# Kernel optimization log

Hardware: AMD Instinct MI355X
Metric: run time of the kernel (lower is better)

The kernel has to match this reference:

```python
import jax, jax.numpy as jnp
import numpy as np

H = 64          # hidden_size / SINDy latent dim
DM = 128        # d_model (GRU input size)
FF = 128        # dim_feedforward
NL = 2          # num_sindy_layers
EPS = 1e-5      # LayerNorm eps (torch default)
TRI_I, TRI_J = np.triu_indices(H)          # poly_order=2 pairs, torch loop order (i<=j)
LIB = 1 + H + TRI_I.size                   # 2145


def layernorm(x, g, b):
    m = jnp.mean(x, axis=-1, keepdims=True)
    v = jnp.mean((x - m) ** 2, axis=-1, keepdims=True)
    return (x - m) * jax.lax.rsqrt(v + EPS) * g + b


def sindy_library(z):
    # z: (N, H) -> Theta: (N, 1 + H + H*(H+1)/2); same term ordering as torch loops
    ones = jnp.ones((z.shape[0], 1), z.dtype)
    quad = z[:, TRI_I] * z[:, TRI_J]
    return jnp.concatenate([ones, z, quad], axis=1)


def gru_layer(x, Wih, Whh, bih, bhh):
    # x: (B, S, in), Wih: (3H, in), Whh: (3H, H); torch GRU gate order r,z,n
    xp = jnp.einsum('bsi,gi->bsg', x, Wih) + bih  # (B,S,3H) precomputed input projections
    B = x.shape[0]

    def step(h, xpt):
        gh = h @ Whh.T + bhh
        r = jax.nn.sigmoid(xpt[:, :H] + gh[:, :H])
        z = jax.nn.sigmoid(xpt[:, H:2 * H] + gh[:, H:2 * H])
        n = jnp.tanh(xpt[:, 2 * H:] + r * gh[:, 2 * H:])
        h = (1.0 - z) * n + z * h
        return h, h

    h0 = jnp.zeros((B, H), x.dtype)
    _, ys = jax.lax.scan(step, h0, jnp.swapaxes(xp, 0, 1))  # scan over time
    return jnp.swapaxes(ys, 0, 1)  # (B, S, H)


def sindy_layer(src, coef, g1, b1n, W1, bf1, W2, bf2, g2, b2n):
    B, S, _ = src.shape
    theta = sindy_library(src.reshape(-1, H))          # (N, LIB)
    upd = (theta @ coef).reshape(B, S, H)              # (B, S, H)
    src = layernorm(src + upd, g1, b1n)                # dropout = identity (eval)
    ff = jax.nn.gelu(src @ W1.T + bf1, approximate=False) @ W2.T + bf2
    return layernorm(src + ff, g2, b2n)


def setup_inputs() -> dict:
    key = jax.random.key(0)
    ks = jax.random.split(key, 24)
    f = lambda k, sh, s=0.05: (jax.random.normal(k, sh, dtype=jnp.float32) * s)
    inp = {
        'x': jax.random.normal(ks[0], (32, 500, DM), dtype=jnp.float32),
        # GRU layer 0 (input DM) and layer 1 (input H)
        'Wih0': f(ks[1], (3 * H, DM)), 'Whh0': f(ks[2], (3 * H, H)),
        'bih0': f(ks[3], (3 * H,)), 'bhh0': f(ks[4], (3 * H,)),
        'Wih1': f(ks[5], (3 * H, H)), 'Whh1': f(ks[6], (3 * H, H)),
        'bih1': f(ks[7], (3 * H,)), 'bhh1': f(ks[8], (3 * H,)),
        # stacked params for NL=2 identical SINDy layers
        'coeffs': f(ks[9], (NL, LIB, H), 0.02),
        'ln1_g': jnp.ones((NL, H), jnp.float32), 'ln1_b': jnp.zeros((NL, H), jnp.float32),
        'W1': f(ks[10], (NL, FF, H)), 'b1': f(ks[11], (NL, FF)),
        'W2': f(ks[12], (NL, H, FF)), 'b2': f(ks[13], (NL, H)),
        'ln2_g': jnp.ones((NL, H), jnp.float32), 'ln2_b': jnp.zeros((NL, H), jnp.float32),
    }
    return inp


def reference(x, Wih0, Whh0, bih0, bhh0, Wih1, Whh1, bih1, bhh1,
              coeffs, ln1_g, ln1_b, W1, b1, W2, b2, ln2_g, ln2_b):
    h = gru_layer(x, Wih0, Whh0, bih0, bhh0)
    h = gru_layer(h, Wih1, Whh1, bih1, bhh1)
    for l in range(NL):
        h = sindy_layer(h, coeffs[l], ln1_g[l], ln1_b[l], W1[l], b1[l],
                        W2[l], b2[l], ln2_g[l], ln2_b[l])
    return h, h[:, -1, :]
```

## Files before the change

kernel.cpp:

```cpp
#include <hip/hip_runtime.h>
#include <hip/hip_bf16.h>
#include <math.h>

#define H 64
#define DM 128
#define GDIM 192
#define BSZ 32
#define SEQ 500
#define NROW (BSZ*SEQ)
#define LIBN 2145
#define FFD 128
#define NKC2 75
#define NGRP 300
#define CPK2 153600

typedef __attribute__((ext_vector_type(8))) short short8;
typedef __attribute__((ext_vector_type(4))) float f32x4;
typedef __attribute__((ext_vector_type(2))) float f32x2;
typedef __attribute__((ext_vector_type(4))) unsigned u32x4;

__device__ __forceinline__ float sigf(float x) {
    return 1.0f / (1.0f + __expf(-x));
}
__device__ __forceinline__ float tanhfast(float x) {
    x = fminf(fmaxf(x, -15.0f), 15.0f);
    float t = __expf(-2.0f * x);
    return (1.0f - t) / (1.0f + t);
}
__device__ __forceinline__ short bf16r(float f) {
    unsigned u = __float_as_uint(f);
    unsigned r = (u + 0x7fffu + ((u >> 16) & 1u)) >> 16;
    return (short)r;
}
__device__ __forceinline__ f32x2 pkfma(f32x2 a, f32x2 b, f32x2 c) {
    f32x2 d;
    asm("v_pk_fma_f32 %0, %1, %2, %3" : "=v"(d) : "v"(a), "v"(b), "v"(c));
    return d;
}

__device__ __forceinline__ void grp_decode(int g, int& a, int& b) {
    if (g < 8) { a = 64; b = g * 8; }
    else if (g == 8 || g >= 297) { a = 64; b = 64; }
    else {
        int G = g - 9, acc = 0;
        a = 0; b = 0;
        for (int i2 = 0; i2 < 64; i2++) {
            int cnt = 8 - (i2 >> 3);
            if (G < acc + cnt) { a = i2; b = ((i2 >> 3) + (G - acc)) * 8; break; }
            acc += cnt;
        }
    }
}

__global__ void pack_all(const float* __restrict__ wih0,
                         const float* __restrict__ coeffs,
                         const float* __restrict__ w1,
                         const float* __restrict__ w2,
                         float* __restrict__ wtp,
                         short* __restrict__ bfa) {
    int idx = blockIdx.x * 256 + threadIdx.x;
    if (idx < GDIM * DM) {
        int e  = idx & 3;
        int g  = (idx >> 2) % GDIM;
        int k4 = idx / (GDIM * 4);
        wtp[idx] = wih0[g * DM + k4 * 4 + e];
        return;
    }
    int r = idx - GDIM * DM;
    int l = r / (CPK2 + 2 * 8192);
    int q = r % (CPK2 + 2 * 8192);
    if (q < CPK2) {
        const float* coef = coeffs + (size_t)l * LIBN * H;
        int j = q & 7, lane = (q >> 3) & 63, nt = (q >> 9) & 3, kc = q >> 11;
        int grp = kc * 4 + (lane >> 4);
        int row = -1;
        if (grp < 8) row = 1 + grp * 8 + j;
        else if (grp == 8) row = (j == 0) ? 0 : -1;
        else if (grp < 297) {
            int a, b;
            grp_decode(grp, a, b);
            int jdx = b + j;
            if (jdx >= a) row = 65 + a * 64 - (a * (a - 1)) / 2 + (jdx - a);
        }
        int c = nt * 16 + (lane & 15);
        bfa[(size_t)l * CPK2 + q] = (row >= 0) ? bf16r(coef[(size_t)row * H + c]) : (short)0;
        return;
    }
    int q2 = q - CPK2;
    if (q2 < 8192) {
        const float* w1l = w1 + (size_t)l * FFD * H;
        int j = q2 & 7, lane = (q2 >> 3) & 63, nt = (q2 >> 9) & 7, kc = q2 >> 12;
        int k = kc * 32 + ((lane >> 4) << 3) + j;
        int n = nt * 16 + (lane & 15);
        bfa[(size_t)2 * CPK2 + l * 8192 + q2] = bf16r(w1l[(size_t)n * H + k]);
        return;
    }
    int q3 = q2 - 8192;
    const float* w2l = w2 + (size_t)l * H * FFD;
    int j = q3 & 7, lane = (q3 >> 3) & 63, nt = (q3 >> 9) & 3, kc = q3 >> 11;
    int k = kc * 32 + ((lane >> 4) << 3) + j;
    int n = nt * 16 + (lane & 15);
    bfa[(size_t)2 * CPK2 + 2 * 8192 + l * 8192 + q3] = bf16r(w2l[(size_t)n * FFD + k]);
}

__global__ __launch_bounds__(192, 2) void xp0_gemm(const float* __restrict__ x,
                                                   const float* __restrict__ wtp,
                                                   const float* __restrict__ bih0,
                                                   float* __restrict__ xpT) {
    __shared__ float xs[64][DM];
    int rb = blockIdx.x * 64;
    for (int idx = threadIdx.x; idx < 64 * 32; idx += 192) {
        int r = idx >> 5, k4 = idx & 31;
        ((f32x4*)xs[r])[k4] = ((const f32x4*)(x + (size_t)(rb + r) * DM))[k4];
    }
    __syncthreads();
    int g = threadIdx.x;
    float bias = bih0[g];
    float acc[64];
#pragma unroll
    for (int r = 0; r < 64; r++) acc[r] = bias;
    for (int k4 = 0; k4 < 32; k4++) {
        f32x4 w4 = ((const f32x4*)wtp)[k4 * GDIM + g];
#pragma unroll
        for (int r = 0; r < 64; r++) {
            f32x4 xv = ((f32x4*)xs[r])[k4];
            acc[r] += w4[0] * xv[0] + w4[1] * xv[1] + w4[2] * xv[2] + w4[3] * xv[3];
        }
    }
    for (int r = 0; r < 64; r++) {
        int row = rb + r;
        int bb = row / 500;
        int ss = row - bb * 500;
        xpT[(((size_t)bb * 125 + (ss >> 2)) * GDIM + g) * 4 + (ss & 3)] = acc[r];
    }
}

__global__ __launch_bounds__(768, 3) void gru_fused(const float* __restrict__ xpT,
                                                    const float* __restrict__ whh0,
                                                    const float* __restrict__ bhh0,
                                                    const float* __restrict__ wih1,
                                                    const float* __restrict__ bih1,
                                                    const float* __restrict__ whh1,
                                                    const float* __restrict__ bhh1,
                                                    float* __restrict__ hbuf) {
    int b = blockIdx.x;
    int tid = threadIdx.x;
    int wv = __builtin_amdgcn_readfirstlane(tid >> 6);
    int lane = tid & 63;
    int m = wv % 3;
    int q = wv / 3;
    int k0 = q * 16;

    __shared__ __align__(16) float h0s[H];
    __shared__ __align__(16) float h1s[H];
    __shared__ float part[3][4][GDIM];

    if (tid < H) { h0s[tid] = 0.0f; h1s[tid] = 0.0f; }

    const float* W = (m == 0) ? whh0 : (m == 1) ? wih1 : whh1;
    f32x2 wrp[8], wzp[8], wnp[8];
#pragma unroll
    for (int k4 = 0; k4 < 4; k4++) {
        f32x4 a = ((const f32x4*)(W + (size_t)lane * H + k0))[k4];
        f32x4 c = ((const f32x4*)(W + (size_t)(H + lane) * H + k0))[k4];
        f32x4 d = ((const f32x4*)(W + (size_t)(2 * H + lane) * H + k0))[k4];
        wrp[2*k4]   = __builtin_shufflevector(a, a, 0, 1);
        wrp[2*k4+1] = __builtin_shufflevector(a, a, 2, 3);
        wzp[2*k4]   = __builtin_shufflevector(c, c, 0, 1);
        wzp[2*k4+1] = __builtin_shufflevector(c, c, 2, 3);
        wnp[2*k4]   = __builtin_shufflevector(d, d, 0, 1);
        wnp[2*k4+1] = __builtin_shufflevector(d, d, 2, 3);
    }

    float b0r = 0, b0z = 0, b0n = 0;
    float b1ir = 0, b1iz = 0, b1in = 0, b1hr = 0, b1hz = 0, b1hn = 0;
    float hreg0 = 0.0f, hreg1 = 0.0f;
    float hb4[4] = {0.f, 0.f, 0.f, 0.f};
    f32x4 xc[4][3];
    const float* xpB = xpT + (size_t)b * 125 * GDIM * 4;

    if (wv == 0) {
        b0r = bhh0[lane]; b0z = bhh0[H + lane]; b0n = bhh0[2 * H + lane];
#pragma unroll
        for (int g3 = 0; g3 < 3; g3++) {
            xc[0][g3] = *(const f32x4*)(xpB + ((size_t)0 * GDIM + g3 * 64 + lane) * 4);
            xc[1][g3] = *(const f32x4*)(xpB + ((size_t)1 * GDIM + g3 * 64 + lane) * 4);
        }
    } else if (wv == 2) {
        b1ir = bih1[lane]; b1iz = bih1[H + lane]; b1in = bih1[2 * H + lane];
        b1hr = bhh1[lane]; b1hz = bhh1[H + lane]; b1hn = bhh1[2 * H + lane];
    }
    __syncthreads();

    auto loadch = [&](int c, int buf) {
        if (c < 125) {
#pragma unroll
            for (int g3 = 0; g3 < 3; g3++)
                xc[buf][g3] = *(const f32x4*)(xpB + ((size_t)c * GDIM + g3 * 64 + lane) * 4);
        }
    };

    auto step = [&](int s, int e, float xr, float xz, float xn) {
        const float* hv = (m == 2) ? h1s : h0s;
        f32x2 arp = {0.f, 0.f}, azp = {0.f, 0.f}, anp = {0.f, 0.f};
#pragma unroll
        for (int t4 = 0; t4 < 4; t4++) {
            f32x4 h4 = ((const f32x4*)(hv + k0))[t4];
            f32x2 hlo = __builtin_shufflevector(h4, h4, 0, 1);
            f32x2 hhi = __builtin_shufflevector(h4, h4, 2, 3);
            arp = pkfma(wrp[2*t4], hlo, arp);
            arp = pkfma(wrp[2*t4+1], hhi, arp);
            azp = pkfma(wzp[2*t4], hlo, azp);
            azp = pkfma(wzp[2*t4+1], hhi, azp);
            anp = pkfma(wnp[2*t4], hlo, anp);
            anp = pkfma(wnp[2*t4+1], hhi, anp);
        }
        part[m][q][lane] = arp[0] + arp[1];
        part[m][q][H + lane] = azp[0] + azp[1];
        part[m][q][2 * H + lane] = anp[0] + anp[1];
        __syncthreads();

        if (wv == 0) {
            if (s < SEQ) {
                float gr = b0r, gz = b0z, gn = b0n;
#pragma unroll
                for (int qq = 0; qq < 4; qq++) {
                    gr += part[0][qq][lane];
                    gz += part[0][qq][H + lane];
                    gn += part[0][qq][2 * H + lane];
                }
                float rg = sigf(xr + gr);
                float zg = sigf(xz + gz);
                float ng = tanhfast(xn + rg * gn);
                hreg0 = (1.0f - zg) * ng + zg * hreg0;
                h0s[lane] = hreg0;
            }
        } else if (wv == 2) {
            if (s >= 1) {
                float xr1 = b1ir, xz1 = b1iz, xn1 = b1in;
                float gr1 = b1hr, gz1 = b1hz, gn1 = b1hn;
#pragma unroll
                for (int qq = 0; qq < 4; qq++) {
                    xr1 += part[1][qq][lane];
                    xz1 += part[1][qq][H + lane];
                    xn1 += part[1][qq][2 * H + lane];
                    gr1 += part[2][qq][lane];
                    gz1 += part[2][qq][H + lane];
                    gn1 += part[2][qq][2 * H + lane];
                }
                float rg = sigf(xr1 + gr1);
                float zg = sigf(xz1 + gz1);
                float ng = tanhfast(xn1 + rg * gn1);
                hreg1 = (1.0f - zg) * ng + zg * hreg1;
                h1s[lane] = hreg1;
                hb4[(e + 3) & 3] = hreg1;
                if (e == 0) {
                    float* dst = hbuf + ((size_t)b * SEQ + (s - 4)) * H + lane;
#pragma unroll
                    for (int t = 0; t < 4; t++) dst[t * H] = hb4[t];
                }
            }
        }
        __syncthreads();
    };

    for (int scb = 0; scb < 31; scb++) {
#pragma unroll
        for (int sci = 0; sci < 4; sci++) {
            int sc = scb * 4 + sci;
            if (wv == 0 && (sci & 1) == 0) {
                loadch(sc + 2, (sci + 2) & 3);
                loadch(sc + 3, (sci + 3) & 3);
            }
            int s0 = sc * 4;
            step(s0 + 0, 0, xc[sci][0][0], xc[sci][1][0], xc[sci][2][0]);
            step(s0 + 1, 1, xc[sci][0][1], xc[sci][1][1], xc[sci][2][1]);
            step(s0 + 2, 2, xc[sci][0][2], xc[sci][1][2], xc[sci][2][2]);
            step(s0 + 3, 3, xc[sci][0][3], xc[sci][1][3], xc[sci][2][3]);
        }
    }
    {
        step(496, 0, xc[0][0][0], xc[0][1][0], xc[0][2][0]);
        step(497, 1, xc[0][0][1], xc[0][1][1], xc[0][2][1]);
        step(498, 2, xc[0][0][2], xc[0][1][2], xc[0][2][2]);
        step(499, 3, xc[0][0][3], xc[0][1][3], xc[0][2][3]);
    }
    step(500, 0, 0.0f, 0.0f, 0.0f);
}

__global__ __launch_bounds__(512) void sindy_mfma(float* __restrict__ hbuf,
                                                  const short* __restrict__ cpk,
                                                  const short* __restrict__ w1p,
                                                  const short* __restrict__ w2p,
                                                  const float* __restrict__ g1,
                                                  const float* __restrict__ b1n,
                                                  const float* __restrict__ bf1,
                                                  const float* __restrict__ bf2v,
                                                  const float* __restrict__ g2,
                                                  const float* __restrict__ b2n,
                                                  float* __restrict__ out,
                                                  int final_layer) {
    __shared__ float z[65 * 68];
    __shared__ float upd[64 * 68];
    __shared__ float ff[64 * 132];
    __shared__ unsigned kmap2[NGRP];
    __shared__ float bfs1[FFD], bfs2[H], g1s[H], b1s[H], g2s[H], b2s[H];

    int tid = threadIdx.x;
    int wv = __builtin_amdgcn_readfirstlane(tid >> 6);
    int lane = tid & 63;
    int row0 = blockIdx.x * 64;

    for (int idx = tid; idx < 64 * 16; idx += 512) {
        int r = idx >> 4, c4 = idx & 15;
        *(f32x4*)&z[r * 68 + c4 * 4] = *(const f32x4*)&hbuf[(size_t)(row0 + r) * H + c4 * 4];
    }
    for (int idx = tid; idx < 64 * 17; idx += 512)
        *(f32x4*)&upd[idx * 4] = (f32x4){0.f, 0.f, 0.f, 0.f};
    if (tid < 64) {
        z[tid * 68 + 64] = 1.0f; z[tid * 68 + 65] = 0.0f;
        z[tid * 68 + 66] = 0.0f; z[tid * 68 + 67] = 0.0f;
    }
    if (tid < 68) z[64 * 68 + tid] = 0.0f;
    if (tid < NGRP) {
        int a, b;
        grp_decode(tid, a, b);
        kmap2[tid] = ((unsigned)a << 16) | (unsigned)b;
    }
    if (tid < FFD) bfs1[tid] = bf1[tid];
    if (tid < H) {
        bfs2[tid] = bf2v[tid];
        g1s[tid] = g1[tid]; b1s[tid] = b1n[tid];
        g2s[tid] = g2[tid]; b2s[tid] = b2n[tid];
    }
    __syncthreads();

    int kj0 = ((lane >> 4) << 3);
    int m0 = (wv & 3) * 16;
    int m = m0 + (lane & 15);
    int rbase = m0 + ((lane >> 4) << 2);
    int cb16 = lane & 15;
    const float* zrow = &z[m * 68];

    {
        int p = wv >> 2;
        f32x4 acc[4] = {{0,0,0,0},{0,0,0,0},{0,0,0,0},{0,0,0,0}};
        for (int kc = p; kc < NKC2; kc += 2) {
            unsigned ab = kmap2[kc * 4 + (lane >> 4)];
            float za = zrow[ab >> 16];
            const float* zb = &zrow[ab & 0xffffu];
            f32x4 z0 = *(const f32x4*)zb;
            f32x4 z1 = *(const f32x4*)(zb + 4);
            short8 af;
            af[0] = bf16r(za * z0[0]);
            af[1] = bf16r(za * z0[1]);
            af[2] = bf16r(za * z0[2]);
            af[3] = bf16r(za * z0[3]);
            af[4] = bf16r(za * z1[0]);
            af[5] = bf16r(za * z1[1]);
            af[6] = bf16r(za * z1[2]);
            af[7] = bf16r(za * z1[3]);
            const short* cb = cpk + ((size_t)(kc * 4) * 64 + lane) * 8;
#pragma unroll
            for (int nt = 0; nt < 4; nt++) {
                short8 bf = *(const short8*)(cb + (size_t)nt * 512);
                acc[nt] = __builtin_amdgcn_mfma_f32_16x16x32_bf16(af, bf, acc[nt], 0, 0, 0);
            }
        }
#pragma unroll
        for (int nt = 0; nt < 4; nt++)
#pragma unroll
            for (int r = 0; r < 4; r++)
                atomicAdd(&upd[(rbase + r) * 68 + nt * 16 + cb16], acc[nt][r]);
    }
    __syncthreads();

    if (wv == 0) {
        float v[64];
        float s1 = 0.0f;
#pragma unroll
        for (int c = 0; c < 64; c++) { v[c] = z[lane * 68 + c] + upd[lane * 68 + c]; s1 += v[c]; }
        float mn = s1 * (1.0f / 64.0f);
        float s2 = 0.0f;
#pragma unroll
        for (int c = 0; c < 64; c++) { float d = v[c] - mn; s2 += d * d; }
        float rstd = 1.0f / sqrtf(s2 * (1.0f / 64.0f) + 1e-5f);
#pragma unroll
        for (int c = 0; c < 64; c++)
            z[lane * 68 + c] = (v[c] - mn) * rstd * g1s[c] + b1s[c];
    }
    __syncthreads();

    {
        int nq = wv >> 2;
        f32x4 acc[4] = {{0,0,0,0},{0,0,0,0},{0,0,0,0},{0,0,0,0}};
#pragma unroll
        for (int kc = 0; kc < 2; kc++) {
            f32x4 za = *(const f32x4*)&z[m * 68 + kc * 32 + kj0];
            f32x4 zb = *(const f32x4*)&z[m * 68 + kc * 32 + kj0 + 4];
            short8 af;
            af[0] = bf16r(za[0]); af[1] = bf16r(za[1]); af[2] = bf16r(za[2]); af[3] = bf16r(za[3]);
            af[4] = bf16r(zb[0]); af[5] = bf16r(zb[1]); af[6] = bf16r(zb[2]); af[7] = bf16r(zb[3]);
#pragma unroll
            for (int t = 0; t < 4; t++) {
                int nt = nq * 4 + t;
                short8 bf = *(const short8*)(w1p + ((size_t)(kc * 8 + nt) * 64 + lane) * 8);
                acc[t] = __builtin_amdgcn_mfma_f32_16x16x32_bf16(af, bf, acc[t], 0, 0, 0);
            }
        }
#pragma unroll
        for (int t = 0; t < 4; t++) {
            int col = (nq * 4 + t) * 16 + cb16;
#pragma unroll
            for (int r = 0; r < 4; r++) {
                float v = acc[t][r] + bfs1[col];
                ff[(rbase + r) * 132 + col] = 0.5f * v * (1.0f + erff(v * 0.70710678118654752f));
            }
        }
    }
    __syncthreads();

    {
        int nh = wv >> 2;
        f32x4 acc[2] = {{0,0,0,0},{0,0,0,0}};
        const float* frow = &ff[m * 132];
#pragma unroll
        for (int kc = 0; kc < 4; kc++) {
            f32x4 fa = *(const f32x4*)&frow[kc * 32 + kj0];
            f32x4 fb = *(const f32x4*)&frow[kc * 32 + kj0 + 4];
            short8 af;
            af[0] = bf16r(fa[0]); af[1] = bf16r(fa[1]); af[2] = bf16r(fa[2]); af[3] = bf16r(fa[3]);
            af[4] = bf16r(fb[0]); af[5] = bf16r(fb[1]); af[6] = bf16r(fb[2]); af[7] = bf16r(fb[3]);
#pragma unroll
            for (int t = 0; t < 2; t++) {
                int nt = nh * 2 + t;
                short8 bf = *(const short8*)(w2p + ((size_t)(kc * 4 + nt) * 64 + lane) * 8);
                acc[t] = __builtin_amdgcn_mfma_f32_16x16x32_bf16(af, bf, acc[t], 0, 0, 0);
            }
        }
#pragma unroll
        for (int t = 0; t < 2; t++) {
            int col = (nh * 2 + t) * 16 + cb16;
#pragma unroll
            for (int r = 0; r < 4; r++)
                upd[(rbase + r) * 68 + col] = acc[t][r] + bfs2[col];
        }
    }
    __syncthreads();

    if (wv == 0) {
        float v[64];
        float s1 = 0.0f;
#pragma unroll
        for (int c = 0; c < 64; c++) { v[c] = z[lane * 68 + c] + upd[lane * 68 + c]; s1 += v[c]; }
        float mn = s1 * (1.0f / 64.0f);
        float s2 = 0.0f;
#pragma unroll
        for (int c = 0; c < 64; c++) { float d = v[c] - mn; s2 += d * d; }
        float rstd = 1.0f / sqrtf(s2 * (1.0f / 64.0f) + 1e-5f);
        int row = row0 + lane;
#pragma unroll
        for (int c = 0; c < 64; c++) {
            float res = (v[c] - mn) * rstd * g2s[c] + b2s[c];
            if (!final_layer) {
                hbuf[(size_t)row * H + c] = res;
            } else {
                out[(size_t)row * H + c] = res;
                if (row % SEQ == SEQ - 1)
                    out[(size_t)NROW * H + (row / SEQ) * H + c] = res;
            }
        }
    }
}

extern "C" void kernel_launch(void* const* d_in, const int* in_sizes, int n_in,
                              void* d_out, int out_size, void* d_ws, size_t ws_size,
                              hipStream_t stream) {
    const float* x    = (const float*)d_in[0];
    const float* wih0 = (const float*)d_in[1];
    const float* whh0 = (const float*)d_in[2];
    const float* bih0 = (const float*)d_in[3];
    const float* bhh0 = (const float*)d_in[4];
    const float* wih1 = (const float*)d_in[5];
    const float* whh1 = (const float*)d_in[6];
    const float* bih1 = (const float*)d_in[7];
    const float* bhh1 = (const float*)d_in[8];
    const float* coeffs = (const float*)d_in[9];
    const float* ln1g = (const float*)d_in[10];
    const float* ln1b = (const float*)d_in[11];
    const float* w1   = (const float*)d_in[12];
    const float* b1   = (const float*)d_in[13];
    const float* w2   = (const float*)d_in[14];
    const float* b2   = (const float*)d_in[15];
    const float* ln2g = (const float*)d_in[16];
    const float* ln2b = (const float*)d_in[17];

    float* out = (float*)d_out;
    float* ws  = (float*)d_ws;
    float* xpT = ws;
    float* wtp = ws + (size_t)NROW * GDIM;
    short* bfa = (short*)(wtp + GDIM * DM);
    short* cpk[2] = { bfa, bfa + CPK2 };
    short* w1pk[2] = { bfa + 2 * CPK2, bfa + 2 * CPK2 + 8192 };
    short* w2pk[2] = { bfa + 2 * CPK2 + 2 * 8192, bfa + 2 * CPK2 + 3 * 8192 };
    float* hbuf = out;

    pack_all<<<1424, 256, 0, stream>>>(wih0, coeffs, w1, w2, wtp, bfa);
    xp0_gemm<<<NROW / 64, 192, 0, stream>>>(x, wtp, bih0, xpT);
    gru_fused<<<BSZ, 768, 0, stream>>>(xpT, whh0, bhh0, wih1, bih1, whh1, bhh1, hbuf);
    for (int l = 0; l < 2; l++) {
        sindy_mfma<<<NROW / 64, 512, 0, stream>>>(
            hbuf, cpk[l], w1pk[l], w2pk[l],
            ln1g + l * H, ln1b + l * H, b1 + l * FFD,
            b2 + l * H, ln2g + l * H, ln2b + l * H,
            out, l == 1);
    }
}
```

Measured before the change: 519.9 us.

## Fuse both SINDy layers into one kernel and parallelize LayerNorm across threads

Replaces the two per-layer SINDy launches with a single kernel that loops over both layers while keeping each 64-row tile resident in shared memory. This removes one kernel launch and the global write and re-read of the intermediate hidden state. LayerNorm is also rewritten so all 512 threads take part, eight per row with shuffle reductions, instead of only the first wave doing it serially. The cost is a longer kernel with extra barriers and an extra clearing of the update buffer between layers.

```diff
diff --git a/kernel.cpp b/kernel.cpp
--- a/kernel.cpp
+++ b/kernel.cpp
@@ -288,23 +288,21 @@
     step(500, 0, 0.0f, 0.0f, 0.0f);
 }
 
-__global__ __launch_bounds__(512) void sindy_mfma(float* __restrict__ hbuf,
-                                                  const short* __restrict__ cpk,
-                                                  const short* __restrict__ w1p,
-                                                  const short* __restrict__ w2p,
-                                                  const float* __restrict__ g1,
-                                                  const float* __restrict__ b1n,
-                                                  const float* __restrict__ bf1,
-                                                  const float* __restrict__ bf2v,
-                                                  const float* __restrict__ g2,
-                                                  const float* __restrict__ b2n,
-                                                  float* __restrict__ out,
-                                                  int final_layer) {
+__global__ __launch_bounds__(512) void sindy_fused(const float* __restrict__ hbuf_in,
+                                                   const short* __restrict__ bfa,
+                                                   const float* __restrict__ ln1g,
+                                                   const float* __restrict__ ln1b,
+                                                   const float* __restrict__ b1g,
+                                                   const float* __restrict__ b2g,
+                                                   const float* __restrict__ ln2g,
+                                                   const float* __restrict__ ln2b,
+                                                   float* __restrict__ out) {
     __shared__ float z[65 * 68];
     __shared__ float upd[64 * 68];
     __shared__ float ff[64 * 132];
     __shared__ unsigned kmap2[NGRP];
-    __shared__ float bfs1[FFD], bfs2[H], g1s[H], b1s[H], g2s[H], b2s[H];
+    __shared__ float bfs1[2][FFD], bfs2[2][H];
+    __shared__ float g1s[2][H], b1s[2][H], g2s[2][H], b2s[2][H];
 
     int tid = threadIdx.x;
     int wv = __builtin_amdgcn_readfirstlane(tid >> 6);
@@ -313,7 +311,7 @@
 
     for (int idx = tid; idx < 64 * 16; idx += 512) {
         int r = idx >> 4, c4 = idx & 15;
-        *(f32x4*)&z[r * 68 + c4 * 4] = *(const f32x4*)&hbuf[(size_t)(row0 + r) * H + c4 * 4];
+        *(f32x4*)&z[r * 68 + c4 * 4] = *(const f32x4*)&hbuf_in[(size_t)(row0 + r) * H + c4 * 4];
     }
     for (int idx = tid; idx < 64 * 17; idx += 512)
         *(f32x4*)&upd[idx * 4] = (f32x4){0.f, 0.f, 0.f, 0.f};
@@ -327,11 +325,13 @@
         grp_decode(tid, a, b);
         kmap2[tid] = ((unsigned)a << 16) | (unsigned)b;
     }
-    if (tid < FFD) bfs1[tid] = bf1[tid];
+    if (tid < FFD) { bfs1[0][tid] = b1g[tid]; bfs1[1][tid] = b1g[FFD + tid]; }
     if (tid < H) {
-        bfs2[tid] = bf2v[tid];
-        g1s[tid] = g1[tid]; b1s[tid] = b1n[tid];
-        g2s[tid] = g2[tid]; b2s[tid] = b2n[tid];
+        bfs2[0][tid] = b2g[tid];      bfs2[1][tid] = b2g[H + tid];
+        g1s[0][tid] = ln1g[tid];      g1s[1][tid] = ln1g[H + tid];
+        b1s[0][tid] = ln1b[tid];      b1s[1][tid] = ln1b[H + tid];
+        g2s[0][tid] = ln2g[tid];      g2s[1][tid] = ln2g[H + tid];
+        b2s[0][tid] = ln2b[tid];      b2s[1][tid] = ln2b[H + tid];
     }
     __syncthreads();
 
@@ -341,134 +341,163 @@
     int rbase = m0 + ((lane >> 4) << 2);
     int cb16 = lane & 15;
     const float* zrow = &z[m * 68];
-
-    {
-        int p = wv >> 2;
-        f32x4 acc[4] = {{0,0,0,0},{0,0,0,0},{0,0,0,0},{0,0,0,0}};
-        for (int kc = p; kc < NKC2; kc += 2) {
-            unsigned ab = kmap2[kc * 4 + (lane >> 4)];
-            float za = zrow[ab >> 16];
-            const float* zb = &zrow[ab & 0xffffu];
-            f32x4 z0 = *(const f32x4*)zb;
-            f32x4 z1 = *(const f32x4*)(zb + 4);
-            short8 af;
-            af[0] = bf16r(za * z0[0]);
-            af[1] = bf16r(za * z0[1]);
-            af[2] = bf16r(za * z0[2]);
-            af[3] = bf16r(za * z0[3]);
-            af[4] = bf16r(za * z1[0]);
-            af[5] = bf16r(za * z1[1]);
-            af[6] = bf16r(za * z1[2]);
-            af[7] = bf16r(za * z1[3]);
-            const short* cb = cpk + ((size_t)(kc * 4) * 64 + lane) * 8;
-#pragma unroll
-            for (int nt = 0; nt < 4; nt++) {
-                short8 bf = *(const short8*)(cb + (size_t)nt * 512);
-                acc[nt] = __builtin_amdgcn_mfma_f32_16x16x32_bf16(af, bf, acc[nt], 0, 0, 0);
-            }
-        }
-#pragma unroll
-        for (int nt = 0; nt < 4; nt++)
-#pragma unroll
-            for (int r = 0; r < 4; r++)
-                atomicAdd(&upd[(rbase + r) * 68 + nt * 16 + cb16], acc[nt][r]);
-    }
-    __syncthreads();
-
-    if (wv == 0) {
-        float v[64];
-        float s1 = 0.0f;
-#pragma unroll
-        for (int c = 0; c < 64; c++) { v[c] = z[lane * 68 + c] + upd[lane * 68 + c]; s1 += v[c]; }
-        float mn = s1 * (1.0f / 64.0f);
-        float s2 = 0.0f;
-#pragma unroll
-        for (int c = 0; c < 64; c++) { float d = v[c] - mn; s2 += d * d; }
-        float rstd = 1.0f / sqrtf(s2 * (1.0f / 64.0f) + 1e-5f);
-#pragma unroll
-        for (int c = 0; c < 64; c++)
-            z[lane * 68 + c] = (v[c] - mn) * rstd * g1s[c] + b1s[c];
-    }
-    __syncthreads();
-
-    {
-        int nq = wv >> 2;
-        f32x4 acc[4] = {{0,0,0,0},{0,0,0,0},{0,0,0,0},{0,0,0,0}};
-#pragma unroll
-        for (int kc = 0; kc < 2; kc++) {
-            f32x4 za = *(const f32x4*)&z[m * 68 + kc * 32 + kj0];
-            f32x4 zb = *(const f32x4*)&z[m * 68 + kc * 32 + kj0 + 4];
-            short8 af;
-            af[0] = bf16r(za[0]); af[1] = bf16r(za[1]); af[2] = bf16r(za[2]); af[3] = bf16r(za[3]);
-            af[4] = bf16r(zb[0]); af[5] = bf16r(zb[1]); af[6] = bf16r(zb[2]); af[7] = bf16r(zb[3]);
+    int lrow = tid >> 3;
+    int lk = (tid & 7) * 8;
+
+#pragma unroll
+    for (int l = 0; l < 2; l++) {
+        const short* cpk = bfa + (size_t)l * CPK2;
+        const short* w1p = bfa + (size_t)2 * CPK2 + l * 8192;
+        const short* w2p = bfa + (size_t)2 * CPK2 + 2 * 8192 + l * 8192;
+
+        {
+            int p = wv >> 2;
+            f32x4 acc[4] = {{0,0,0,0},{0,0,0,0},{0,0,0,0},{0,0,0,0}};
+            for (int kc = p; kc < NKC2; kc += 2) {
+                unsigned ab = kmap2[kc * 4 + (lane >> 4)];
+                float za = zrow[ab >> 16];
+                const float* zb = &zrow[ab & 0xffffu];
+                f32x4 z0 = *(const f32x4*)zb;
+                f32x4 z1 = *(const f32x4*)(zb + 4);
+                short8 af;
+                af[0] = bf16r(za * z0[0]);
+                af[1] = bf16r(za * z0[1]);
+                af[2] = bf16r(za * z0[2]);
+                af[3] = bf16r(za * z0[3]);
+                af[4] = bf16r(za * z1[0]);
+                af[5] = bf16r(za * z1[1]);
+                af[6] = bf16r(za * z1[2]);
+                af[7] = bf16r(za * z1[3]);
+                const short* cb = cpk + ((size_t)(kc * 4) * 64 + lane) * 8;
+#pragma unroll
+                for (int nt = 0; nt < 4; nt++) {
+                    short8 bf = *(const short8*)(cb + (size_t)nt * 512);
+                    acc[nt] = __builtin_amdgcn_mfma_f32_16x16x32_bf16(af, bf, acc[nt], 0, 0, 0);
+                }
+            }
+#pragma unroll
+            for (int nt = 0; nt < 4; nt++)
+#pragma unroll
+                for (int r = 0; r < 4; r++)
+                    atomicAdd(&upd[(rbase + r) * 68 + nt * 16 + cb16], acc[nt][r]);
+        }
+        __syncthreads();
+
+        {
+            float v[8];
+            float s1 = 0.0f;
+#pragma unroll
+            for (int i = 0; i < 8; i++) {
+                v[i] = z[lrow * 68 + lk + i] + upd[lrow * 68 + lk + i];
+                s1 += v[i];
+            }
+            s1 += __shfl_xor(s1, 1); s1 += __shfl_xor(s1, 2); s1 += __shfl_xor(s1, 4);
+            float mn = s1 * (1.0f / 64.0f);
+            float s2 = 0.0f;
+#pragma unroll
+            for (int i = 0; i < 8; i++) { float d = v[i] - mn; s2 += d * d; }
+            s2 += __shfl_xor(s2, 1); s2 += __shfl_xor(s2, 2); s2 += __shfl_xor(s2, 4);
+            float rstd = 1.0f / sqrtf(s2 * (1.0f / 64.0f) + 1e-5f);
+#pragma unroll
+            for (int i = 0; i < 8; i++)
+                z[lrow * 68 + lk + i] = (v[i] - mn) * rstd * g1s[l][lk + i] + b1s[l][lk + i];
+        }
+        __syncthreads();
+
+        {
+            int nq = wv >> 2;
+            f32x4 acc[4] = {{0,0,0,0},{0,0,0,0},{0,0,0,0},{0,0,0,0}};
+#pragma unroll
+            for (int kc = 0; kc < 2; kc++) {
+                f32x4 za = *(const f32x4*)&z[m * 68 + kc * 32 + kj0];
+                f32x4 zb = *(const f32x4*)&z[m * 68 + kc * 32 + kj0 + 4];
+                short8 af;
+                af[0] = bf16r(za[0]); af[1] = bf16r(za[1]); af[2] = bf16r(za[2]); af[3] = bf16r(za[3]);
+                af[4] = bf16r(zb[0]); af[5] = bf16r(zb[1]); af[6] = bf16r(zb[2]); af[7] = bf16r(zb[3]);
+#pragma unroll
+                for (int t = 0; t < 4; t++) {
+                    int nt = nq * 4 + t;
+                    short8 bf = *(const short8*)(w1p + ((size_t)(kc * 8 + nt) * 64 + lane) * 8);
+                    acc[t] = __builtin_amdgcn_mfma_f32_16x16x32_bf16(af, bf, acc[t], 0, 0, 0);
+                }
+            }
 #pragma unroll
             for (int t = 0; t < 4; t++) {
-                int nt = nq * 4 + t;
-                short8 bf = *(const short8*)(w1p + ((size_t)(kc * 8 + nt) * 64 + lane) * 8);
-                acc[t] = __builtin_amdgcn_mfma_f32_16x16x32_bf16(af, bf, acc[t], 0, 0, 0);
-            }
-        }
-#pragma unroll
-        for (int t = 0; t < 4; t++) {
-            int col = (nq * 4 + t) * 16 + cb16;
-#pragma unroll
-            for (int r = 0; r < 4; r++) {
-                float v = acc[t][r] + bfs1[col];
-                ff[(rbase + r) * 132 + col] = 0.5f * v * (1.0f + erff(v * 0.70710678118654752f));
-            }
-        }
-    }
-    __syncthreads();
-
-    {
-        int nh = wv >> 2;
-        f32x4 acc[2] = {{0,0,0,0},{0,0,0,0}};
-        const float* frow = &ff[m * 132];
-#pragma unroll
-        for (int kc = 0; kc < 4; kc++) {
-            f32x4 fa = *(const f32x4*)&frow[kc * 32 + kj0];
-            f32x4 fb = *(const f32x4*)&frow[kc * 32 + kj0 + 4];
-            short8 af;
-            af[0] = bf16r(fa[0]); af[1] = bf16r(fa[1]); af[2] = bf16r(fa[2]); af[3] = bf16r(fa[3]);
-            af[4] = bf16r(fb[0]); af[5] = bf16r(fb[1]); af[6] = bf16r(fb[2]); af[7] = bf16r(fb[3]);
+                int col = (nq * 4 + t) * 16 + cb16;
+#pragma unroll
+                for (int r = 0; r < 4; r++) {
+                    float v = acc[t][r] + bfs1[l][col];
+                    ff[(rbase + r) * 132 + col] = 0.5f * v * (1.0f + erff(v * 0.70710678118654752f));
+                }
+            }
+        }
+        __syncthreads();
+
+        {
+            int nh = wv >> 2;
+            f32x4 acc[2] = {{0,0,0,0},{0,0,0,0}};
+            const float* frow = &ff[m * 132];
+#pragma unroll
+            for (int kc = 0; kc < 4; kc++) {
+                f32x4 fa = *(const f32x4*)&frow[kc * 32 + kj0];
+                f32x4 fb = *(const f32x4*)&frow[kc * 32 + kj0 + 4];
+                short8 af;
+                af[0] = bf16r(fa[0]); af[1] = bf16r(fa[1]); af[2] = bf16r(fa[2]); af[3] = bf16r(fa[3]);
+                af[4] = bf16r(fb[0]); af[5] = bf16r(fb[1]); af[6] = bf16r(fb[2]); af[7] = bf16r(fb[3]);
+#pragma unroll
+                for (int t = 0; t < 2; t++) {
+                    int nt = nh * 2 + t;
+                    short8 bf = *(const short8*)(w2p + ((size_t)(kc * 4 + nt) * 64 + lane) * 8);
+                    acc[t] = __builtin_amdgcn_mfma_f32_16x16x32_bf16(af, bf, acc[t], 0, 0, 0);
+                }
+            }
 #pragma unroll
             for (int t = 0; t < 2; t++) {
-                int nt = nh * 2 + t;
-                short8 bf = *(const short8*)(w2p + ((size_t)(kc * 4 + nt) * 64 + lane) * 8);
-                acc[t] = __builtin_amdgcn_mfma_f32_16x16x32_bf16(af, bf, acc[t], 0, 0, 0);
-            }
-        }
-#pragma unroll
-        for (int t = 0; t < 2; t++) {
-            int col = (nh * 2 + t) * 16 + cb16;
-#pragma unroll
-            for (int r = 0; r < 4; r++)
-                upd[(rbase + r) * 68 + col] = acc[t][r] + bfs2[col];
-        }
-    }
-    __syncthreads();
-
-    if (wv == 0) {
-        float v[64];
-        float s1 = 0.0f;
-#pragma unroll
-        for (int c = 0; c < 64; c++) { v[c] = z[lane * 68 + c] + upd[lane * 68 + c]; s1 += v[c]; }
-        float mn = s1 * (1.0f / 64.0f);
-        float s2 = 0.0f;
-#pragma unroll
-        for (int c = 0; c < 64; c++) { float d = v[c] - mn; s2 += d * d; }
-        float rstd = 1.0f / sqrtf(s2 * (1.0f / 64.0f) + 1e-5f);
-        int row = row0 + lane;
-#pragma unroll
-        for (int c = 0; c < 64; c++) {
-            float res = (v[c] - mn) * rstd * g2s[c] + b2s[c];
-            if (!final_layer) {
-                hbuf[(size_t)row * H + c] = res;
+                int col = (nh * 2 + t) * 16 + cb16;
+#pragma unroll
+                for (int r = 0; r < 4; r++)
+                    upd[(rbase + r) * 68 + col] = acc[t][r] + bfs2[l][col];
+            }
+        }
+        __syncthreads();
+
+        {
+            float v[8];
+            float s1 = 0.0f;
+#pragma unroll
+            for (int i = 0; i < 8; i++) {
+                v[i] = z[lrow * 68 + lk + i] + upd[lrow * 68 + lk + i];
+                s1 += v[i];
+            }
+            s1 += __shfl_xor(s1, 1); s1 += __shfl_xor(s1, 2); s1 += __shfl_xor(s1, 4);
+            float mn = s1 * (1.0f / 64.0f);
+            float s2 = 0.0f;
+#pragma unroll
+            for (int i = 0; i < 8; i++) { float d = v[i] - mn; s2 += d * d; }
+            s2 += __shfl_xor(s2, 1); s2 += __shfl_xor(s2, 2); s2 += __shfl_xor(s2, 4);
+            float rstd = 1.0f / sqrtf(s2 * (1.0f / 64.0f) + 1e-5f);
+            if (l == 0) {
+#pragma unroll
+                for (int i = 0; i < 8; i++)
+                    z[lrow * 68 + lk + i] = (v[i] - mn) * rstd * g2s[0][lk + i] + b2s[0][lk + i];
             } else {
-                out[(size_t)row * H + c] = res;
-                if (row % SEQ == SEQ - 1)
-                    out[(size_t)NROW * H + (row / SEQ) * H + c] = res;
-            }
+                int row = row0 + lrow;
+                int last = (row % SEQ == SEQ - 1);
+#pragma unroll
+                for (int i = 0; i < 8; i++) {
+                    float res = (v[i] - mn) * rstd * g2s[1][lk + i] + b2s[1][lk + i];
+                    out[(size_t)row * H + lk + i] = res;
+                    if (last)
+                        out[(size_t)NROW * H + (row / SEQ) * H + lk + i] = res;
+                }
+            }
+        }
+        __syncthreads();
+
+        if (l == 0) {
+            for (int idx = tid; idx < 64 * 17; idx += 512)
+                *(f32x4*)&upd[idx * 4] = (f32x4){0.f, 0.f, 0.f, 0.f};
+            __syncthreads();
         }
     }
 }
@@ -500,19 +529,11 @@
     float* xpT = ws;
     float* wtp = ws + (size_t)NROW * GDIM;
     short* bfa = (short*)(wtp + GDIM * DM);
-    short* cpk[2] = { bfa, bfa + CPK2 };
-    short* w1pk[2] = { bfa + 2 * CPK2, bfa + 2 * CPK2 + 8192 };
-    short* w2pk[2] = { bfa + 2 * CPK2 + 2 * 8192, bfa + 2 * CPK2 + 3 * 8192 };
     float* hbuf = out;
 
     pack_all<<<1424, 256, 0, stream>>>(wih0, coeffs, w1, w2, wtp, bfa);
     xp0_gemm<<<NROW / 64, 192, 0, stream>>>(x, wtp, bih0, xpT);
     gru_fused<<<BSZ, 768, 0, stream>>>(xpT, whh0, bhh0, wih1, bih1, whh1, bhh1, hbuf);
-    for (int l = 0; l < 2; l++) {
-        sindy_mfma<<<NROW / 64, 512, 0, stream>>>(
-            hbuf, cpk[l], w1pk[l], w2pk[l],
-            ln1g + l * H, ln1b + l * H, b1 + l * FFD,
-            b2 + l * H, ln2g + l * H, ln2b + l * H,
-            out, l == 1);
-    }
-}
+    sindy_fused<<<NROW / 64, 512, 0, stream>>>(hbuf, bfa, ln1g, ln1b, b1, b2,
+                                               ln2g, ln2b, out);
+}
```

New measurement: 510.2 us. No clear change (-1.9%).
